# Kernel tuning notes

Hardware: AMD Instinct MI355X
Metric: run time of the kernel (lower is better)

Reference implementation:

```python
import jax, jax.numpy as jnp
import numpy as np

N_ROWS = 8192
EMBED_DIM = 256


def setup_inputs() -> dict:
    key = jax.random.key(0)
    k1, k2, k3, k4, k5 = jax.random.split(key, 5)
    M = jax.random.normal(k1, (N_ROWS, EMBED_DIM), dtype=jnp.float32)
    N = jax.random.normal(k2, (N_ROWS, EMBED_DIM), dtype=jnp.float32)
    # gate_w: nn.Linear(embed_dim, 1) -> weight [1, d], bias [1]; gate_b extra scalar param [1]
    Wg = jax.random.normal(k3, (1, EMBED_DIM), dtype=jnp.float32) * 0.06
    bg = jax.random.normal(k4, (1,), dtype=jnp.float32) * 0.1
    gate_b = jax.random.normal(k5, (1,), dtype=jnp.float32) * 0.1
    return {"M": M, "N": N, "Wg": Wg, "bg": bg, "gate_b": gate_b, "iseval": 0}


def reference(M, N, Wg, bg, gate_b, iseval):
    # mt: [n, n] cross-similarity scores
    mt = jnp.matmul(N, M.T)
    if not iseval:
        # training branch: zero out the diagonal (mt - diag(diag(mt)))
        n = mt.shape[0]
        idx = jnp.arange(n)
        mt = mt.at[idx, idx].set(0.0)
    else:
        # eval branch: zero out the first row
        mt = mt.at[0].set(0.0)
    attn_weight = jax.nn.softmax(mt, axis=-1)          # [n, n]
    out_attn = jnp.matmul(attn_weight, M)              # [n, d]
    gate = jax.nn.sigmoid(jnp.matmul(out_attn, Wg.T) + bg + gate_b)  # [n, 1]
    boosted = out_attn * gate + N * (1.0 - gate)       # [n, d]
    return boosted[:, None, None, :]                   # [n, 1, 1, d]
```

## Files before the change

kernel.cpp:

```cpp
#include <hip/hip_runtime.h>


constexpr int EMBED = 256;
constexpr int BQ = 64;
constexpr int BJ = 32;
constexpr int NT = 256;
constexpr int NS = 8;

constexpr int SS_OFF = 0;
constexpr int PH_OFF = 18432;
constexpr int MS_OFF = 23552;
constexpr int LS_OFF = 23808;
constexpr int AS_OFF = 24064;
constexpr int LDS_SZ = 24320;

typedef _Float16 half8 __attribute__((ext_vector_type(8)));
typedef float f32x4 __attribute__((ext_vector_type(4)));
typedef short short8v __attribute__((ext_vector_type(8)));

static __device__ __forceinline__ f32x4 mfma16(half8 a, half8 b, f32x4 c) {
    return __builtin_amdgcn_mfma_f32_16x16x32_f16(a, b, c, 0, 0, 0);
}
static __device__ __forceinline__ short f2h(float x) {
    return (short)__builtin_bit_cast(unsigned short, (_Float16)x);
}

__global__ void prep(const float* __restrict__ M,
                     short* __restrict__ MhG, short* __restrict__ MtG) {
    __shared__ float L[16 * 260];
    const int r0 = blockIdx.x * 16;
    const int t = threadIdx.x;
    const int pj = t >> 4, pc = (t & 15) * 16;
    {
        const float* src = M + (size_t)(r0 + pj) * EMBED + pc;
        float4 v[4];
        #pragma unroll
        for (int i = 0; i < 4; ++i) v[i] = ((const float4*)src)[i];
        short* hd = MhG + (size_t)(r0 + pj) * EMBED + pc;
        #pragma unroll
        for (int i = 0; i < 2; ++i) {
            float4 a = v[2 * i], b = v[2 * i + 1];
            short8v h;
            h[0]=f2h(a.x); h[1]=f2h(a.y); h[2]=f2h(a.z); h[3]=f2h(a.w);
            h[4]=f2h(b.x); h[5]=f2h(b.y); h[6]=f2h(b.z); h[7]=f2h(b.w);
            *(short8v*)(hd + 8 * i) = h;
        }
        #pragma unroll
        for (int i = 0; i < 4; ++i)
            *(float4*)(L + pj * 260 + pc + 4 * i) = v[i];
    }
    __syncthreads();
    {
        const int d = t;
        const int tile = r0 >> 5, jh = (r0 >> 4) & 1;
        short* dst = MtG + (size_t)tile * (BJ * EMBED) + d * BJ + jh * 16;
        #pragma unroll
        for (int g2 = 0; g2 < 2; ++g2) {
            short8v w;
            #pragma unroll
            for (int e = 0; e < 8; ++e) w[e] = f2h(L[(g2 * 8 + e) * 260 + d]);
            *(short8v*)(dst + g2 * 8) = w;
        }
    }
}

__launch_bounds__(NT, 2)
__global__ void attn(const short* __restrict__ MhG, const short* __restrict__ MtG,
                     const float* __restrict__ Ng, const int* __restrict__ iseval_p,
                     float* __restrict__ O0out, short* __restrict__ Ofp,
                     float* __restrict__ MLm, float* __restrict__ MLl, int n)
{
    __shared__ __align__(16) char smem[LDS_SZ];
    float* MS = (float*)(smem + MS_OFF);
    float* LS = (float*)(smem + LS_OFF);
    float* AS = (float*)(smem + AS_OFF);

    const int t = threadIdx.x, lane = t & 63, wave = t >> 6;
    const int quad = lane >> 4, mn = lane & 15;
    const int bid = blockIdx.x;
    const int s  = bid & (NS - 1);
    const int qb = bid >> 3;
    const int q0 = qb * BQ;
    const int jbase = s * (n / NS);
    const int jb32 = jbase / BJ;
    const int ntiles = (n / NS) / BJ;
    const int iseval = *iseval_p;
    const int jt = wave & 1, kh = wave >> 1;
    const int dq = wave;
    const int sq = t >> 2, sh = t & 3;

    if (t < BQ) { MS[t] = -1e30f; LS[t] = 0.f; }

    half8 Qf[4][4];
    #pragma unroll
    for (int qi = 0; qi < 4; ++qi) {
        const float* np = Ng + (size_t)(q0 + qi * 16 + mn) * EMBED;
        #pragma unroll
        for (int kk = 0; kk < 4; ++kk) {
            const float* p = np + (kh * 4 + kk) * 32 + quad * 8;
            float4 a = *(const float4*)p, b = *(const float4*)(p + 4);
            half8 h;
            h[0]=(_Float16)a.x; h[1]=(_Float16)a.y; h[2]=(_Float16)a.z; h[3]=(_Float16)a.w;
            h[4]=(_Float16)b.x; h[5]=(_Float16)b.y; h[6]=(_Float16)b.z; h[7]=(_Float16)b.w;
            Qf[qi][kk] = h;
        }
    }

    f32x4 O[4][4];
    #pragma unroll
    for (int qi = 0; qi < 4; ++qi)
        #pragma unroll
        for (int dt = 0; dt < 4; ++dt) O[qi][dt] = (f32x4){0.f, 0.f, 0.f, 0.f};

    const short* mhb0 = MhG + (size_t)(jbase + jt * 16 + mn) * EMBED + kh * 128 + quad * 8;
    half8 Bc[4], Bn[4], Mtf[4];
    #pragma unroll
    for (int kk = 0; kk < 4; ++kk) Bc[kk] = *(const half8*)(mhb0 + kk * 32);

    __syncthreads();

    for (int tile = 0; tile < ntiles; ++tile) {
        const int j0g = jbase + tile * BJ;

        {
            f32x4 a0 = (f32x4){0,0,0,0}, a1 = (f32x4){0,0,0,0};
            f32x4 a2 = (f32x4){0,0,0,0}, a3 = (f32x4){0,0,0,0};
            #pragma unroll
            for (int kk = 0; kk < 4; ++kk) {
                half8 bf = Bc[kk];
                a0 = mfma16(Qf[0][kk], bf, a0);
                a1 = mfma16(Qf[1][kk], bf, a1);
                a2 = mfma16(Qf[2][kk], bf, a2);
                a3 = mfma16(Qf[3][kk], bf, a3);
            }
            float* ssp = (float*)(smem + SS_OFF) + kh * 2304;
            #pragma unroll
            for (int r = 0; r < 4; ++r) {
                ssp[(0  + quad * 4 + r) * 36 + jt * 16 + mn] = a0[r];
                ssp[(16 + quad * 4 + r) * 36 + jt * 16 + mn] = a1[r];
                ssp[(32 + quad * 4 + r) * 36 + jt * 16 + mn] = a2[r];
                ssp[(48 + quad * 4 + r) * 36 + jt * 16 + mn] = a3[r];
            }
        }
        __syncthreads();

        if (tile + 1 < ntiles) {
            const short* nb = mhb0 + (size_t)(tile + 1) * (BJ * EMBED);
            #pragma unroll
            for (int kk = 0; kk < 4; ++kk) Bn[kk] = *(const half8*)(nb + kk * 32);
        }
        {
            const short* mtb = MtG + (size_t)(jb32 + tile) * (BJ * EMBED);
            #pragma unroll
            for (int dt = 0; dt < 4; ++dt)
                Mtf[dt] = *(const half8*)(mtb + (dq * 64 + dt * 16 + mn) * BJ + quad * 8);
        }

        {
            const float* p0 = (const float*)(smem + SS_OFF) + sq * 36 + 8 * sh;
            float4 sa = *(const float4*)p0;
            float4 sb = *(const float4*)(p0 + 4);
            float4 sc = *(const float4*)(p0 + 2304);
            float4 sd = *(const float4*)(p0 + 2308);
            float sv[8] = {sa.x + sc.x, sa.y + sc.y, sa.z + sc.z, sa.w + sc.w,
                           sb.x + sd.x, sb.y + sd.y, sb.z + sd.z, sb.w + sd.w};
            const int qg = q0 + sq;
            if (iseval) {
                if (qg == 0) {
                    #pragma unroll
                    for (int i = 0; i < 8; ++i) sv[i] = 0.f;
                }
            } else {
                int dj = qg - j0g - 8 * sh;
                #pragma unroll
                for (int i = 0; i < 8; ++i) if (dj == i) sv[i] = 0.f;
            }
            float mx = sv[0];
            #pragma unroll
            for (int i = 1; i < 8; ++i) mx = fmaxf(mx, sv[i]);
            mx = fmaxf(mx, __shfl_xor(mx, 1));
            mx = fmaxf(mx, __shfl_xor(mx, 2));
            float m_old = MS[sq];
            float m_new = fmaxf(m_old, mx);
            float alpha = __expf(m_old - m_new);
            float p[8], ps = 0.f;
            #pragma unroll
            for (int i = 0; i < 8; ++i) { p[i] = __expf(sv[i] - m_new); ps += p[i]; }
            ps += __shfl_xor(ps, 1);
            ps += __shfl_xor(ps, 2);
            if (sh == 0) {
                MS[sq] = m_new;
                AS[sq] = alpha;
                LS[sq] = LS[sq] * alpha + ps;
            }
            half8 ph;
            #pragma unroll
            for (int i = 0; i < 8; ++i) ph[i] = (_Float16)p[i];
            *(half8*)(smem + PH_OFF + sq * 80 + sh * 16) = ph;
        }
        __syncthreads();

        #pragma unroll
        for (int qi = 0; qi < 4; ++qi) {
            half8 pf = *(const half8*)(smem + PH_OFF + (qi * 16 + mn) * 80 + quad * 16);
            f32x4 al = *(const f32x4*)((const float*)(smem + AS_OFF) + qi * 16 + quad * 4);
            #pragma unroll
            for (int dt = 0; dt < 4; ++dt) {
                f32x4 o = O[qi][dt];
                o[0] *= al[0]; o[1] *= al[1]; o[2] *= al[2]; o[3] *= al[3];
                O[qi][dt] = mfma16(pf, Mtf[dt], o);
            }
        }
        #pragma unroll
        for (int kk = 0; kk < 4; ++kk) Bc[kk] = Bn[kk];
    }

    if (s == 0) {
        #pragma unroll
        for (int qi = 0; qi < 4; ++qi)
            #pragma unroll
            for (int dt = 0; dt < 4; ++dt) {
                int col = dq * 64 + dt * 16 + mn;
                #pragma unroll
                for (int r = 0; r < 4; ++r)
                    O0out[(size_t)(q0 + qi * 16 + quad * 4 + r) * EMBED + col] = O[qi][dt][r];
            }
    } else {
        short* dst = Ofp + (size_t)(s - 1) * n * EMBED;
        #pragma unroll
        for (int qi = 0; qi < 4; ++qi)
            #pragma unroll
            for (int dt = 0; dt < 4; ++dt) {
                int col = dq * 64 + dt * 16 + mn;
                #pragma unroll
                for (int r = 0; r < 4; ++r)
                    dst[(size_t)(q0 + qi * 16 + quad * 4 + r) * EMBED + col] = f2h(O[qi][dt][r]);
            }
    }
    if (t < BQ) {
        MLm[s * n + q0 + t] = MS[t];
        MLl[s * n + q0 + t] = LS[t];
    }
}

__global__ void combine8(const float* __restrict__ O0, const short* __restrict__ Ofp,
                         const float* __restrict__ MLm, const float* __restrict__ MLl,
                         const float* __restrict__ Ng, const float* __restrict__ Wg,
                         const float* __restrict__ bg, const float* __restrict__ gb,
                         float* __restrict__ out, int n)
{
    const int t = threadIdx.x;
    const int row = blockIdx.x * 16 + (t >> 4);
    const int c = t & 15;
    float ms[NS], ls[NS];
    #pragma unroll
    for (int k = 0; k < NS; ++k) { ms[k] = MLm[k * n + row]; ls[k] = MLl[k * n + row]; }
    float m = ms[0];
    #pragma unroll
    for (int k = 1; k < NS; ++k) m = fmaxf(m, ms[k]);
    float w[NS], lsum = 0.f;
    #pragma unroll
    for (int k = 0; k < NS; ++k) { w[k] = __expf(ms[k] - m); lsum += w[k] * ls[k]; }
    float linv = 1.f / lsum;

    float acc[16];
    {
        const float4* o0 = (const float4*)(O0 + (size_t)row * EMBED + c * 16);
        #pragma unroll
        for (int i = 0; i < 4; ++i) {
            float4 v = o0[i];
            acc[4*i+0] = w[0] * v.x; acc[4*i+1] = w[0] * v.y;
            acc[4*i+2] = w[0] * v.z; acc[4*i+3] = w[0] * v.w;
        }
    }
    #pragma unroll
    for (int k = 1; k < NS; ++k) {
        const short* op = Ofp + (size_t)(k - 1) * n * EMBED + (size_t)row * EMBED + c * 16;
        half8 a = *(const half8*)op, b = *(const half8*)(op + 8);
        #pragma unroll
        for (int i = 0; i < 8; ++i) {
            acc[i]     += w[k] * (float)a[i];
            acc[8 + i] += w[k] * (float)b[i];
        }
    }
    float dot = 0.f;
    #pragma unroll
    for (int i = 0; i < 16; ++i) { acc[i] *= linv; dot += acc[i] * Wg[c * 16 + i]; }
    dot += __shfl_xor(dot, 1);
    dot += __shfl_xor(dot, 2);
    dot += __shfl_xor(dot, 4);
    dot += __shfl_xor(dot, 8);
    float g = 1.f / (1.f + __expf(-(dot + bg[0] + gb[0])));
    const float4* n4 = (const float4*)(Ng + (size_t)row * EMBED + c * 16);
    float4* o4 = (float4*)(out + (size_t)row * EMBED + c * 16);
    #pragma unroll
    for (int i = 0; i < 4; ++i) {
        float4 nn = n4[i];
        float4 res;
        res.x = acc[4*i+0] * g + nn.x * (1.f - g);
        res.y = acc[4*i+1] * g + nn.y * (1.f - g);
        res.z = acc[4*i+2] * g + nn.z * (1.f - g);
        res.w = acc[4*i+3] * g + nn.w * (1.f - g);
        o4[i] = res;
    }
}

extern "C" void kernel_launch(void* const* d_in, const int* in_sizes, int n_in,
                              void* d_out, int out_size, void* d_ws, size_t ws_size,
                              hipStream_t stream) {
    const float* M      = (const float*)d_in[0];
    const float* N      = (const float*)d_in[1];
    const float* Wgp    = (const float*)d_in[2];
    const float* bgp    = (const float*)d_in[3];
    const float* gbp    = (const float*)d_in[4];
    const int*   iseval = (const int*)d_in[5];
    float* out = (float*)d_out;

    int n = in_sizes[0] / EMBED;
    short* MhG = (short*)d_ws;
    short* MtG = MhG + (size_t)n * EMBED;
    short* Ofp = MtG + (size_t)n * EMBED;
    float* MLm = (float*)(Ofp + (size_t)(NS - 1) * n * EMBED);
    float* MLl = MLm + (size_t)NS * n;

    hipLaunchKernelGGL(prep, dim3(n / 16), dim3(NT), 0, stream, M, MhG, MtG);
    hipLaunchKernelGGL(attn, dim3((n / BQ) * NS), dim3(NT), 0, stream,
                       MhG, MtG, N, iseval, out, Ofp, MLm, MLl, n);
    hipLaunchKernelGGL(combine8, dim3(n / 16), dim3(NT), 0, stream,
                       out, Ofp, MLm, MLl, N, Wgp, bgp, gbp, out, n);
}
```

Measured before the change: 202.6 us.

## Halve query tile to 32 rows and split keys four ways instead of eight

The attention kernel now processes 32 query rows per block instead of 64 and splits the key range into 4 chunks instead of 8. Block IDs are remapped so pairs of query blocks share a key split, and the softmax stage uses 8 threads per row with 4 scores each. The register double-buffering of the next key tile is dropped in favour of loading it at the top of each iteration. This lowers registers and LDS per block and shrinks the partial-result combine traffic, but each K/V tile is reused across fewer queries and global-load latency is no longer hidden by prefetch.

```diff
diff --git a/kernel.cpp b/kernel.cpp
--- a/kernel.cpp
+++ b/kernel.cpp
@@ -2,17 +2,17 @@
 
 
 constexpr int EMBED = 256;
-constexpr int BQ = 64;
+constexpr int BQ = 32;
 constexpr int BJ = 32;
 constexpr int NT = 256;
-constexpr int NS = 8;
+constexpr int NS = 4;
 
 constexpr int SS_OFF = 0;
-constexpr int PH_OFF = 18432;
-constexpr int MS_OFF = 23552;
-constexpr int LS_OFF = 23808;
-constexpr int AS_OFF = 24064;
-constexpr int LDS_SZ = 24320;
+constexpr int PH_OFF = 9216;
+constexpr int MS_OFF = 11776;
+constexpr int LS_OFF = 11904;
+constexpr int AS_OFF = 12032;
+constexpr int LDS_SZ = 12160;
 
 typedef _Float16 half8 __attribute__((ext_vector_type(8)));
 typedef float f32x4 __attribute__((ext_vector_type(4)));
@@ -78,8 +78,8 @@
     const int t = threadIdx.x, lane = t & 63, wave = t >> 6;
     const int quad = lane >> 4, mn = lane & 15;
     const int bid = blockIdx.x;
-    const int s  = bid & (NS - 1);
-    const int qb = bid >> 3;
+    const int s  = (bid & 7) >> 1;
+    const int qb = ((bid >> 3) << 1) | (bid & 1);
     const int q0 = qb * BQ;
     const int jbase = s * (n / NS);
     const int jb32 = jbase / BJ;
@@ -87,13 +87,13 @@
     const int iseval = *iseval_p;
     const int jt = wave & 1, kh = wave >> 1;
     const int dq = wave;
-    const int sq = t >> 2, sh = t & 3;
+    const int sq = t >> 3, sh = t & 7;
 
     if (t < BQ) { MS[t] = -1e30f; LS[t] = 0.f; }
 
-    half8 Qf[4][4];
-    #pragma unroll
-    for (int qi = 0; qi < 4; ++qi) {
+    half8 Qf[2][4];
+    #pragma unroll
+    for (int qi = 0; qi < 2; ++qi) {
         const float* np = Ng + (size_t)(q0 + qi * 16 + mn) * EMBED;
         #pragma unroll
         for (int kk = 0; kk < 4; ++kk) {
@@ -106,49 +106,44 @@
         }
     }
 
-    f32x4 O[4][4];
-    #pragma unroll
-    for (int qi = 0; qi < 4; ++qi)
+    f32x4 O[2][4];
+    #pragma unroll
+    for (int qi = 0; qi < 2; ++qi)
         #pragma unroll
         for (int dt = 0; dt < 4; ++dt) O[qi][dt] = (f32x4){0.f, 0.f, 0.f, 0.f};
 
     const short* mhb0 = MhG + (size_t)(jbase + jt * 16 + mn) * EMBED + kh * 128 + quad * 8;
-    half8 Bc[4], Bn[4], Mtf[4];
-    #pragma unroll
-    for (int kk = 0; kk < 4; ++kk) Bc[kk] = *(const half8*)(mhb0 + kk * 32);
 
     __syncthreads();
 
     for (int tile = 0; tile < ntiles; ++tile) {
         const int j0g = jbase + tile * BJ;
 
+        half8 Bc[4];
+        {
+            const short* nb = mhb0 + (size_t)tile * (BJ * EMBED);
+            #pragma unroll
+            for (int kk = 0; kk < 4; ++kk) Bc[kk] = *(const half8*)(nb + kk * 32);
+        }
+
         {
             f32x4 a0 = (f32x4){0,0,0,0}, a1 = (f32x4){0,0,0,0};
-            f32x4 a2 = (f32x4){0,0,0,0}, a3 = (f32x4){0,0,0,0};
             #pragma unroll
             for (int kk = 0; kk < 4; ++kk) {
                 half8 bf = Bc[kk];
                 a0 = mfma16(Qf[0][kk], bf, a0);
                 a1 = mfma16(Qf[1][kk], bf, a1);
-                a2 = mfma16(Qf[2][kk], bf, a2);
-                a3 = mfma16(Qf[3][kk], bf, a3);
-            }
-            float* ssp = (float*)(smem + SS_OFF) + kh * 2304;
+            }
+            float* ssp = (float*)(smem + SS_OFF) + kh * 1152;
             #pragma unroll
             for (int r = 0; r < 4; ++r) {
                 ssp[(0  + quad * 4 + r) * 36 + jt * 16 + mn] = a0[r];
                 ssp[(16 + quad * 4 + r) * 36 + jt * 16 + mn] = a1[r];
-                ssp[(32 + quad * 4 + r) * 36 + jt * 16 + mn] = a2[r];
-                ssp[(48 + quad * 4 + r) * 36 + jt * 16 + mn] = a3[r];
             }
         }
         __syncthreads();
 
-        if (tile + 1 < ntiles) {
-            const short* nb = mhb0 + (size_t)(tile + 1) * (BJ * EMBED);
-            #pragma unroll
-            for (int kk = 0; kk < 4; ++kk) Bn[kk] = *(const half8*)(nb + kk * 32);
-        }
+        half8 Mtf[4];
         {
             const short* mtb = MtG + (size_t)(jb32 + tile) * (BJ * EMBED);
             #pragma unroll
@@ -157,51 +152,47 @@
         }
 
         {
-            const float* p0 = (const float*)(smem + SS_OFF) + sq * 36 + 8 * sh;
+            const float* p0 = (const float*)(smem + SS_OFF) + sq * 36 + 4 * sh;
             float4 sa = *(const float4*)p0;
-            float4 sb = *(const float4*)(p0 + 4);
-            float4 sc = *(const float4*)(p0 + 2304);
-            float4 sd = *(const float4*)(p0 + 2308);
-            float sv[8] = {sa.x + sc.x, sa.y + sc.y, sa.z + sc.z, sa.w + sc.w,
-                           sb.x + sd.x, sb.y + sd.y, sb.z + sd.z, sb.w + sd.w};
+            float4 sc = *(const float4*)(p0 + 1152);
+            float sv[4] = {sa.x + sc.x, sa.y + sc.y, sa.z + sc.z, sa.w + sc.w};
             const int qg = q0 + sq;
             if (iseval) {
                 if (qg == 0) {
                     #pragma unroll
-                    for (int i = 0; i < 8; ++i) sv[i] = 0.f;
+                    for (int i = 0; i < 4; ++i) sv[i] = 0.f;
                 }
             } else {
-                int dj = qg - j0g - 8 * sh;
+                int dj = qg - j0g - 4 * sh;
                 #pragma unroll
-                for (int i = 0; i < 8; ++i) if (dj == i) sv[i] = 0.f;
-            }
-            float mx = sv[0];
-            #pragma unroll
-            for (int i = 1; i < 8; ++i) mx = fmaxf(mx, sv[i]);
+                for (int i = 0; i < 4; ++i) if (dj == i) sv[i] = 0.f;
+            }
+            float mx = fmaxf(fmaxf(sv[0], sv[1]), fmaxf(sv[2], sv[3]));
             mx = fmaxf(mx, __shfl_xor(mx, 1));
             mx = fmaxf(mx, __shfl_xor(mx, 2));
+            mx = fmaxf(mx, __shfl_xor(mx, 4));
             float m_old = MS[sq];
             float m_new = fmaxf(m_old, mx);
             float alpha = __expf(m_old - m_new);
-            float p[8], ps = 0.f;
-            #pragma unroll
-            for (int i = 0; i < 8; ++i) { p[i] = __expf(sv[i] - m_new); ps += p[i]; }
+            float p[4], ps = 0.f;
+            #pragma unroll
+            for (int i = 0; i < 4; ++i) { p[i] = __expf(sv[i] - m_new); ps += p[i]; }
             ps += __shfl_xor(ps, 1);
             ps += __shfl_xor(ps, 2);
+            ps += __shfl_xor(ps, 4);
             if (sh == 0) {
                 MS[sq] = m_new;
                 AS[sq] = alpha;
                 LS[sq] = LS[sq] * alpha + ps;
             }
-            half8 ph;
-            #pragma unroll
-            for (int i = 0; i < 8; ++i) ph[i] = (_Float16)p[i];
-            *(half8*)(smem + PH_OFF + sq * 80 + sh * 16) = ph;
+            short4 ph;
+            ph.x = f2h(p[0]); ph.y = f2h(p[1]); ph.z = f2h(p[2]); ph.w = f2h(p[3]);
+            *(short4*)(smem + PH_OFF + sq * 80 + sh * 8) = ph;
         }
         __syncthreads();
 
         #pragma unroll
-        for (int qi = 0; qi < 4; ++qi) {
+        for (int qi = 0; qi < 2; ++qi) {
             half8 pf = *(const half8*)(smem + PH_OFF + (qi * 16 + mn) * 80 + quad * 16);
             f32x4 al = *(const f32x4*)((const float*)(smem + AS_OFF) + qi * 16 + quad * 4);
             #pragma unroll
@@ -211,13 +202,11 @@
                 O[qi][dt] = mfma16(pf, Mtf[dt], o);
             }
         }
-        #pragma unroll
-        for (int kk = 0; kk < 4; ++kk) Bc[kk] = Bn[kk];
     }
 
     if (s == 0) {
         #pragma unroll
-        for (int qi = 0; qi < 4; ++qi)
+        for (int qi = 0; qi < 2; ++qi)
             #pragma unroll
             for (int dt = 0; dt < 4; ++dt) {
                 int col = dq * 64 + dt * 16 + mn;
@@ -228,7 +217,7 @@
     } else {
         short* dst = Ofp + (size_t)(s - 1) * n * EMBED;
         #pragma unroll
-        for (int qi = 0; qi < 4; ++qi)
+        for (int qi = 0; qi < 2; ++qi)
             #pragma unroll
             for (int dt = 0; dt < 4; ++dt) {
                 int col = dq * 64 + dt * 16 + mn;
@@ -243,7 +232,7 @@
     }
 }
 
-__global__ void combine8(const float* __restrict__ O0, const short* __restrict__ Ofp,
+__global__ void combine4(const float* __restrict__ O0, const short* __restrict__ Ofp,
                          const float* __restrict__ MLm, const float* __restrict__ MLl,
                          const float* __restrict__ Ng, const float* __restrict__ Wg,
                          const float* __restrict__ bg, const float* __restrict__ gb,
@@ -326,6 +315,6 @@
     hipLaunchKernelGGL(prep, dim3(n / 16), dim3(NT), 0, stream, M, MhG, MtG);
     hipLaunchKernelGGL(attn, dim3((n / BQ) * NS), dim3(NT), 0, stream,
                        MhG, MtG, N, iseval, out, Ofp, MLm, MLl, n);
-    hipLaunchKernelGGL(combine8, dim3(n / 16), dim3(NT), 0, stream,
+    hipLaunchKernelGGL(combine4, dim3(n / 16), dim3(NT), 0, stream,
                        out, Ofp, MLm, MLl, N, Wgp, bgp, gbp, out, n);
 }
```

Result: slower. 263.8 us (+30.2%).
